# Kernel tuning notes

Hardware: AMD Instinct MI355X
Metric: run time of the kernel (lower is better)

Reference implementation:

```python
import jax, jax.numpy as jnp
import numpy as np

H = 128   # hidden_size
B = 8
TQ = 512  # num queries
TK = 512  # num keys


def setup_inputs() -> dict:
    key = jax.random.key(0)
    ks = jax.random.split(key, 8)
    s = 1.0 / np.sqrt(H)  # torch Linear default init bound
    return {
        "queries": jax.random.normal(ks[0], (B, TQ, H), dtype=jnp.float32),
        "keys": jax.random.normal(ks[1], (B, TK, H), dtype=jnp.float32),
        "Wa_w": jax.random.uniform(ks[2], (H, H), jnp.float32, -s, s),
        "Wa_b": jax.random.uniform(ks[3], (H,), jnp.float32, -s, s),
        "Ua_w": jax.random.uniform(ks[4], (H, H), jnp.float32, -s, s),
        "Ua_b": jax.random.uniform(ks[5], (H,), jnp.float32, -s, s),
        "Va_w": jax.random.uniform(ks[6], (H,), jnp.float32, -s, s),
        "Va_b": jax.random.uniform(ks[7], (), jnp.float32, -s, s),
    }


def reference(queries, keys, Wa_w, Wa_b, Ua_w, Ua_b, Va_w, Va_b):
    # Linear projections (torch Linear: y = x @ W.T + b)
    q = queries @ Wa_w.T + Wa_b                  # (B, Tq, H)
    k = keys @ Ua_w.T + Ua_b                     # (B, Tk, H)
    # Additive (Bahdanau) scores with broadcast intermediate (B, Tq, Tk, H)
    e = jnp.tanh(q[:, :, None, :] + k[:, None, :, :])
    scores = jnp.einsum('bqkh,h->bqk', e, Va_w) + Va_b  # (B, Tq, Tk)
    weights = jax.nn.softmax(scores, axis=-1)            # softmax over keys
    contexts = jnp.einsum('bqk,bkh->bqh', weights, keys) # (B, Tq, H)
    return contexts, weights
```

## Files before the change

### kernel.cpp

```cpp
#include <hip/hip_runtime.h>
#include <hip/hip_bf16.h>
#include <stdint.h>

#define HD 128
#define NB 8
#define TQN 512
#define TKN 512
#define QT 8
#define KTILE 64
#define KSTR 132
#define QSTR 132
#define KBSTR 136

typedef __attribute__((ext_vector_type(8))) short short8;
typedef __attribute__((ext_vector_type(4))) float f32x4;

static __device__ __forceinline__ float lo16(uint32_t w){
  union { uint32_t i; float f; } v; v.i = w << 16; return v.f;
}
static __device__ __forceinline__ float hi16(uint32_t w){
  union { uint32_t i; float f; } v; v.i = w & 0xffff0000u; return v.f;
}
static __device__ __forceinline__ float bf2f(unsigned short u){
  union { uint32_t i; float f; } v; v.i = ((uint32_t)u) << 16; return v.f;
}
static __device__ __forceinline__ uint32_t f2bf(float f){
  union { float f; uint32_t i; } v; v.f = f;
  uint32_t u = v.i;
  u += 0x7fffu + ((u >> 16) & 1u);
  return u >> 16;
}

static __device__ __forceinline__ float ld1(const void* p, size_t idx, bool f32){
  return f32 ? ((const float*)p)[idx] : bf2f(((const unsigned short*)p)[idx]);
}
static __device__ __forceinline__ short8 ld8bf(const void* p, size_t idx, bool f32){
  short8 r;
  if (f32){
    const float* s = (const float*)p + idx;
    #pragma unroll
    for (int i = 0; i < 8; i++) r[i] = (short)f2bf(s[i]);
  } else {
    r = *(const short8*)((const unsigned short*)p + idx);
  }
  return r;
}

static __device__ __forceinline__ void stage_keys(const void* keys, bool fK,
    unsigned short* keys_s, int b, int kt, int tid){
  if (fK){
    const float4* src = (const float4*)((const float*)keys + (size_t)(b*TKN + kt*KTILE)*HD);
    #pragma unroll
    for (int j = 0; j < 4; j++){
      const int f = tid + 512*j;
      float4 v = src[f];
      const int k = f >> 5;
      const int h = (f & 31) * 4;
      uint2 p;
      p.x = f2bf(v.x) | (f2bf(v.y) << 16);
      p.y = f2bf(v.z) | (f2bf(v.w) << 16);
      *(uint2*)(keys_s + k*KBSTR + h) = p;
    }
  } else {
    const uint4* src = (const uint4*)((const unsigned short*)keys + (size_t)(b*TKN + kt*KTILE)*HD);
    #pragma unroll
    for (int j = 0; j < 2; j++){
      const int f = tid + 512*j;
      uint4 v = src[f];
      const int k = f >> 4;
      const int h = (f & 15) * 8;
      *(uint4*)(keys_s + k*KBSTR + h) = v;
    }
  }
}

__global__ __launch_bounds__(512, 4) void fused_kernel(
    const void* __restrict__ queries, const void* __restrict__ keys,
    const void* __restrict__ Wa_w,   const void* __restrict__ Wa_b,
    const void* __restrict__ Ua_w,   const void* __restrict__ Ua_b,
    const void* __restrict__ Va_w,
    void* __restrict__ out)
{
  __shared__ float qp_s[QT*QSTR];
  __shared__ float va_s[HD];
  __shared__ __align__(16) unsigned short keys_s[KTILE*KBSTR];
  __shared__ __align__(16) float kp_s[KTILE*KSTR];
  __shared__ float sc_s[QT*TKN];
  __shared__ unsigned int flg_s[8];

  const int tid = threadIdx.x;

  if (tid < 8) flg_s[tid] = 0;
  __syncthreads();
  {
    const void* ptrs[7] = {queries, keys, Wa_w, Wa_b, Ua_w, Ua_b, Va_w};
    const int grp = tid >> 5;
    const int l   = tid & 31;
    if (grp < 7){
      const unsigned short* p = (const unsigned short*)ptrs[grp];
      unsigned short a = p[2*l];
      unsigned short c = p[64 + 2*l];
      if (((a >> 7) & 0xFF) > 0x90 || ((c >> 7) & 0xFF) > 0x90)
        atomicOr(&flg_s[grp], 1u);
    }
  }
  __syncthreads();
  const bool fQ  = flg_s[0] != 0;
  const bool fK  = flg_s[1] != 0;
  const bool fWw = flg_s[2] != 0;
  const bool fWb = flg_s[3] != 0;
  const bool fUw = flg_s[4] != 0;
  const bool fUb = flg_s[5] != 0;
  const bool fVw = flg_s[6] != 0;

  const int lane = tid & 63;
  const int wv   = tid >> 6;
  const int ln   = lane & 15;
  const int quad = lane >> 4;
  const int b     = blockIdx.x >> 6;
  const int qbase = (blockIdx.x & 63) * QT;
  const float Cs = 2.8853900817779268f;

  if (tid < HD) va_s[tid] = ld1(Va_w, tid, fVw);

  {
    const int h0 = wv * 16;
    const size_t qrow = (size_t)(b*TQN + qbase + (ln & 7))*HD;
    f32x4 c = {0.f,0.f,0.f,0.f};
    #pragma unroll
    for (int ks = 0; ks < 4; ks++){
      short8 a = ld8bf(queries, qrow + ks*32 + quad*8, fQ);
      short8 w = ld8bf(Wa_w, (size_t)(h0 + ln)*HD + ks*32 + quad*8, fWw);
      c = __builtin_amdgcn_mfma_f32_16x16x32_bf16(a, w, c, 0,0,0);
    }
    const float wb = ld1(Wa_b, h0 + ln, fWb);
    #pragma unroll
    for (int r = 0; r < 4; r++){
      const int row = quad*4 + r;
      if (row < QT) qp_s[row*QSTR + h0 + ln] = (c[r] + wb)*Cs;
    }
  }

  short8 ub[4];
  float ubias;
  {
    const int h0 = wv * 16;
    #pragma unroll
    for (int ks = 0; ks < 4; ks++)
      ub[ks] = ld8bf(Ua_w, (size_t)(h0 + ln)*HD + ks*32 + quad*8, fUw);
    ubias = ld1(Ua_b, h0 + ln, fUb);
  }

  stage_keys(keys, fK, keys_s, b, 0, tid);
  __syncthreads();

  float S0 = 0.f;
  #pragma unroll 8
  for (int h = 0; h < HD; h++) S0 += va_s[h];

  const float4* q4p = (const float4*)(qp_s + wv*QSTR);
  const float4* v4p = (const float4*)va_s;

  for (int kt = 0; kt < 8; kt++){
    f32x4 kc[4];
    #pragma unroll
    for (int mt = 0; mt < 4; mt++) kc[mt] = (f32x4){0.f,0.f,0.f,0.f};
    #pragma unroll
    for (int ks = 0; ks < 4; ks++){
      short8 af[4];
      #pragma unroll
      for (int mt = 0; mt < 4; mt++)
        af[mt] = *(const short8*)(keys_s + (mt*16 + ln)*KBSTR + ks*32 + quad*8);
      #pragma unroll
      for (int mt = 0; mt < 4; mt++)
        kc[mt] = __builtin_amdgcn_mfma_f32_16x16x32_bf16(af[mt], ub[ks], kc[mt], 0,0,0);
    }
    __syncthreads();

    #pragma unroll
    for (int mt = 0; mt < 4; mt++)
      #pragma unroll
      for (int r = 0; r < 4; r++)
        kp_s[(mt*16 + quad*4 + r)*KSTR + wv*16 + ln] = (kc[mt][r] + ubias)*Cs;
    if (kt < 7) stage_keys(keys, fK, keys_s, b, kt+1, tid);
    __syncthreads();

    float acc = 0.f;
    const float4* krow4 = (const float4*)(kp_s + lane*KSTR);
    #pragma unroll 8
    for (int hh = 0; hh < 32; hh++){
      const float4 kv = krow4[hh];
      const float4 qv = q4p[hh];
      const float4 vv = v4p[hh];
      float r0 = __builtin_amdgcn_rcpf(__builtin_amdgcn_exp2f(qv.x + kv.x) + 1.f);
      float r1 = __builtin_amdgcn_rcpf(__builtin_amdgcn_exp2f(qv.y + kv.y) + 1.f);
      float r2 = __builtin_amdgcn_rcpf(__builtin_amdgcn_exp2f(qv.z + kv.z) + 1.f);
      float r3 = __builtin_amdgcn_rcpf(__builtin_amdgcn_exp2f(qv.w + kv.w) + 1.f);
      acc = fmaf(vv.x, r0, acc);
      acc = fmaf(vv.y, r1, acc);
      acc = fmaf(vv.z, r2, acc);
      acc = fmaf(vv.w, r3, acc);
    }
    sc_s[wv*TKN + kt*KTILE + lane] = S0 - 2.f*acc;
  }
  __syncthreads();

  {
    float vals[8];
    float m = -1e30f;
    #pragma unroll
    for (int j = 0; j < 8; j++){
      vals[j] = sc_s[wv*TKN + lane + 64*j];
      m = fmaxf(m, vals[j]);
    }
    #pragma unroll
    for (int o = 32; o > 0; o >>= 1) m = fmaxf(m, __shfl_xor(m, o));
    float sum = 0.f;
    #pragma unroll
    for (int j = 0; j < 8; j++){
      vals[j] = __builtin_amdgcn_exp2f((vals[j]-m)*1.4426950408889634f);
      sum += vals[j];
    }
    #pragma unroll
    for (int o = 32; o > 0; o >>= 1) sum += __shfl_xor(sum, o);
    const float inv = 1.f / sum;
    const size_t wbase = (size_t)NB*TQN*HD + (size_t)(b*TQN + qbase + wv)*TKN;
    #pragma unroll
    for (int j = 0; j < 8; j++){
      const float w = vals[j]*inv;
      sc_s[wv*TKN + lane + 64*j] = w;
      if (fQ) ((float*)out)[wbase + lane + 64*j] = w;
      else    ((unsigned short*)out)[wbase + lane + 64*j] = (unsigned short)f2bf(w);
    }
  }
  __syncthreads();

  {
    const int h0 = ln * 8;
    float a[8];
    #pragma unroll
    for (int t = 0; t < 8; t++) a[t] = 0.f;
    for (int kt = 0; kt < 8; kt++){
      if (fK){
        const float4* src = (const float4*)((const float*)keys + (size_t)(b*TKN + kt*KTILE)*HD);
        #pragma unroll
        for (int j = 0; j < 4; j++){
          const int f = tid + 512*j;
          const int k = f >> 5;
          const int h = (f & 31) * 4;
          *(float4*)(kp_s + k*KSTR + h) = src[f];
        }
      } else {
        const uint4* src = (const uint4*)((const unsigned short*)keys + (size_t)(b*TKN + kt*KTILE)*HD);
        #pragma unroll
        for (int j = 0; j < 2; j++){
          const int f = tid + 512*j;
          const int k = f >> 4;
          const int h = (f & 15) * 8;
          uint4 v = src[f];
          float4 d0, d1;
          d0.x = lo16(v.x); d0.y = hi16(v.x); d0.z = lo16(v.y); d0.w = hi16(v.y);
          d1.x = lo16(v.z); d1.y = hi16(v.z); d1.z = lo16(v.w); d1.w = hi16(v.w);
          *(float4*)(kp_s + k*KSTR + h)     = d0;
          *(float4*)(kp_s + k*KSTR + h + 4) = d1;
        }
      }
      __syncthreads();
      const float* wr = sc_s + wv*TKN + kt*KTILE;
      #pragma unroll 4
      for (int i = 0; i < 16; i++){
        const int k = 4*i + quad;
        const float w = wr[k];
        const float4 k0 = *(const float4*)(kp_s + k*KSTR + h0);
        const float4 k1 = *(const float4*)(kp_s + k*KSTR + h0 + 4);
        a[0] = fmaf(w, k0.x, a[0]); a[1] = fmaf(w, k0.y, a[1]);
        a[2] = fmaf(w, k0.z, a[2]); a[3] = fmaf(w, k0.w, a[3]);
        a[4] = fmaf(w, k1.x, a[4]); a[5] = fmaf(w, k1.y, a[5]);
        a[6] = fmaf(w, k1.z, a[6]); a[7] = fmaf(w, k1.w, a[7]);
      }
      __syncthreads();
    }
    #pragma unroll
    for (int t = 0; t < 8; t++){
      a[t] += __shfl_xor(a[t], 16);
      a[t] += __shfl_xor(a[t], 32);
    }
    if (quad == 0){
      const size_t crow = (size_t)(b*TQN + qbase + wv)*HD + h0;
      if (fQ){
        float* oc = (float*)out;
        *(float4*)(oc + crow)     = (float4){a[0],a[1],a[2],a[3]};
        *(float4*)(oc + crow + 4) = (float4){a[4],a[5],a[6],a[7]};
      } else {
        uint4 o;
        o.x = f2bf(a[0]) | (f2bf(a[1]) << 16);
        o.y = f2bf(a[2]) | (f2bf(a[3]) << 16);
        o.z = f2bf(a[4]) | (f2bf(a[5]) << 16);
        o.w = f2bf(a[6]) | (f2bf(a[7]) << 16);
        *(uint4*)((unsigned short*)out + crow) = o;
      }
    }
  }
}

extern "C" void kernel_launch(void* const* d_in, const int* in_sizes, int n_in,
                              void* d_out, int out_size, void* d_ws, size_t ws_size,
                              hipStream_t stream) {
  (void)in_sizes; (void)n_in; (void)out_size; (void)d_ws; (void)ws_size;
  fused_kernel<<<512, 512, 0, stream>>>(d_in[0], d_in[1], d_in[2], d_in[3],
                                        d_in[4], d_in[5], d_in[6], d_out);
}
```

Measured before the change: 166.2 us.

## Use tanh addition identity to replace per-element exp with rational form

The code now precomputes tanh of the projected queries and keys once, then evaluates tanh(q+k) through the identity (tq+tk)/(1+tq*tk). The reciprocal uses a bit-trick seed with two Newton steps done in ALU. This removes the transcendental exp2 and hardware rcp from the inner O(Tq*Tk*H) loop and keeps only FMA-class arithmetic. The trade-off is more ALU instructions per element and possible accuracy loss when 1+tq*tk approaches zero.

```diff
diff --git a/kernel.cpp b/kernel.cpp
--- a/kernel.cpp
+++ b/kernel.cpp
@@ -29,6 +29,20 @@
   uint32_t u = v.i;
   u += 0x7fffu + ((u >> 16) & 1u);
   return u >> 16;
+}
+
+static __device__ __forceinline__ float fast_rcp(float d){
+  union { float f; uint32_t i; } v; v.f = d;
+  v.i = 0x7EF311C3u - v.i;
+  float y = v.f;
+  y = y * fmaf(-d, y, 2.0f);
+  y = y * fmaf(-d, y, 2.0f);
+  return y;
+}
+
+static __device__ __forceinline__ float tanh_acc(float x){
+  float e = __builtin_amdgcn_exp2f(x * 2.8853900817779268f);
+  return fmaf(-2.0f, fast_rcp(e + 1.0f), 1.0f);
 }
 
 static __device__ __forceinline__ float ld1(const void* p, size_t idx, bool f32){
@@ -119,7 +133,6 @@
   const int quad = lane >> 4;
   const int b     = blockIdx.x >> 6;
   const int qbase = (blockIdx.x & 63) * QT;
-  const float Cs = 2.8853900817779268f;
 
   if (tid < HD) va_s[tid] = ld1(Va_w, tid, fVw);
 
@@ -137,7 +150,7 @@
     #pragma unroll
     for (int r = 0; r < 4; r++){
       const int row = quad*4 + r;
-      if (row < QT) qp_s[row*QSTR + h0 + ln] = (c[r] + wb)*Cs;
+      if (row < QT) qp_s[row*QSTR + h0 + ln] = tanh_acc(c[r] + wb);
     }
   }
 
@@ -153,10 +166,6 @@
 
   stage_keys(keys, fK, keys_s, b, 0, tid);
   __syncthreads();
-
-  float S0 = 0.f;
-  #pragma unroll 8
-  for (int h = 0; h < HD; h++) S0 += va_s[h];
 
   const float4* q4p = (const float4*)(qp_s + wv*QSTR);
   const float4* v4p = (const float4*)va_s;
@@ -181,7 +190,7 @@
     for (int mt = 0; mt < 4; mt++)
       #pragma unroll
       for (int r = 0; r < 4; r++)
-        kp_s[(mt*16 + quad*4 + r)*KSTR + wv*16 + ln] = (kc[mt][r] + ubias)*Cs;
+        kp_s[(mt*16 + quad*4 + r)*KSTR + wv*16 + ln] = tanh_acc(kc[mt][r] + ubias);
     if (kt < 7) stage_keys(keys, fK, keys_s, b, kt+1, tid);
     __syncthreads();
 
@@ -189,19 +198,19 @@
     const float4* krow4 = (const float4*)(kp_s + lane*KSTR);
     #pragma unroll 8
     for (int hh = 0; hh < 32; hh++){
-      const float4 kv = krow4[hh];
-      const float4 qv = q4p[hh];
+      const float4 tk = krow4[hh];
+      const float4 tq = q4p[hh];
       const float4 vv = v4p[hh];
-      float r0 = __builtin_amdgcn_rcpf(__builtin_amdgcn_exp2f(qv.x + kv.x) + 1.f);
-      float r1 = __builtin_amdgcn_rcpf(__builtin_amdgcn_exp2f(qv.y + kv.y) + 1.f);
-      float r2 = __builtin_amdgcn_rcpf(__builtin_amdgcn_exp2f(qv.z + kv.z) + 1.f);
-      float r3 = __builtin_amdgcn_rcpf(__builtin_amdgcn_exp2f(qv.w + kv.w) + 1.f);
-      acc = fmaf(vv.x, r0, acc);
-      acc = fmaf(vv.y, r1, acc);
-      acc = fmaf(vv.z, r2, acc);
-      acc = fmaf(vv.w, r3, acc);
-    }
-    sc_s[wv*TKN + kt*KTILE + lane] = S0 - 2.f*acc;
+      float n0 = tq.x + tk.x, d0 = fmaf(tq.x, tk.x, 1.f);
+      float n1 = tq.y + tk.y, d1 = fmaf(tq.y, tk.y, 1.f);
+      float n2 = tq.z + tk.z, d2 = fmaf(tq.z, tk.z, 1.f);
+      float n3 = tq.w + tk.w, d3 = fmaf(tq.w, tk.w, 1.f);
+      acc = fmaf(vv.x, n0*fast_rcp(d0), acc);
+      acc = fmaf(vv.y, n1*fast_rcp(d1), acc);
+      acc = fmaf(vv.z, n2*fast_rcp(d2), acc);
+      acc = fmaf(vv.w, n3*fast_rcp(d3), acc);
+    }
+    sc_s[wv*TKN + kt*KTILE + lane] = acc;
   }
   __syncthreads();
 
```

New measurement: 164.5 us. About the same (-1.0%).
